# Performance work log

Measured on AMD Instinct MI355X. Metric: run time of the kernel, lower is better.

The kernel has to match this reference:

```python
import jax, jax.numpy as jnp
import numpy as np

# dims: L layers, D d_model, H heads, DH head_dim, DFF ffn, V vocab, BLK nf4 blocksize
L, D, H, DH, DFF, V, BLK = 2, 2048, 16, 128, 5504, 32000, 64
B, S, C, T = 4, 1000, 7, 45

# bitsandbytes NF4 codebook (fixed 16 quantiles of N(0,1), normalized to [-1,1])
NF4 = jnp.array([-1.0, -0.6961928009986877, -0.5250730514526367, -0.39491748809814453,
                 -0.28444138169288635, -0.18477343022823334, -0.09105003625154495, 0.0,
                 0.07958029955625534, 0.16093020141124725, 0.24611230194568634,
                 0.3379152417182922, 0.44070982933044434, 0.5626170039176941,
                 0.7229568362236023, 1.0], dtype=jnp.float32)


def _dequant(idx, scale):
    # idx: [out, in] int in [0,16); scale: [out, in//BLK] per-block absmax
    o, i = idx.shape
    return (NF4[idx].reshape(o, i // BLK, BLK) * scale[:, :, None]).reshape(o, i)


def _rmsnorm(h, w, eps=1e-5):
    return h * jax.lax.rsqrt(jnp.mean(h * h, axis=-1, keepdims=True) + eps) * w


def _rot_half(x):
    x1, x2 = jnp.split(x, 2, axis=-1)
    return jnp.concatenate([-x2, x1], axis=-1)


def _llama_fwd(token_ids, embed, wq_idx, wq_scale, wk_idx, wk_scale, wv_idx, wv_scale,
               wo_idx, wo_scale, wg_idx, wg_scale, wu_idx, wu_scale, wd_idx, wd_scale,
               ln1_w, ln2_w, lnf_w):
    Bt, St = token_ids.shape
    h = embed[token_ids]  # [B,S,D]
    # rotary embeddings
    inv = 1.0 / (10000.0 ** (jnp.arange(0, DH, 2, dtype=jnp.float32) / DH))
    ang = jnp.arange(St, dtype=jnp.float32)[:, None] * inv[None, :]  # [S, DH/2]
    emb_ang = jnp.concatenate([ang, ang], axis=-1)  # [S, DH]
    cos, sin = jnp.cos(emb_ang), jnp.sin(emb_ang)
    mask = jnp.where(jnp.tril(jnp.ones((St, St), dtype=bool)), 0.0, -1e9)  # causal
    for l in range(L):
        xn = _rmsnorm(h, ln1_w[l])
        q = (xn @ _dequant(wq_idx[l], wq_scale[l]).T).reshape(Bt, St, H, DH).transpose(0, 2, 1, 3)
        k = (xn @ _dequant(wk_idx[l], wk_scale[l]).T).reshape(Bt, St, H, DH).transpose(0, 2, 1, 3)
        v = (xn @ _dequant(wv_idx[l], wv_scale[l]).T).reshape(Bt, St, H, DH).transpose(0, 2, 1, 3)
        q = q * cos + _rot_half(q) * sin
        k = k * cos + _rot_half(k) * sin
        att = jax.nn.softmax(jnp.einsum('bhqd,bhkd->bhqk', q, k) / np.float32(np.sqrt(DH)) + mask, axis=-1)
        ctx = jnp.einsum('bhqk,bhkd->bhqd', att, v).transpose(0, 2, 1, 3).reshape(Bt, St, D)
        h = h + ctx @ _dequant(wo_idx[l], wo_scale[l]).T
        xn = _rmsnorm(h, ln2_w[l])
        g = xn @ _dequant(wg_idx[l], wg_scale[l]).T
        u = xn @ _dequant(wu_idx[l], wu_scale[l]).T
        h = h + (jax.nn.silu(g) * u) @ _dequant(wd_idx[l], wd_scale[l]).T
    # hidden_states[-1].mean(dim=1)
    return _rmsnorm(h, lnf_w).mean(axis=1)


def setup_inputs() -> dict:
    key = jax.random.key(0)
    ks = jax.random.split(key, 20)
    ridx = lambda k, shp: jax.random.randint(k, shp, 0, 16, dtype=jnp.int32)
    rsc = lambda k, shp: jax.random.uniform(k, shp, minval=0.01, maxval=0.03, dtype=jnp.float32)
    return {
        'x': jax.random.normal(ks[0], (B, C, T), dtype=jnp.float32),
        'token_ids': jax.random.randint(ks[1], (B, S), 0, V, dtype=jnp.int32),
        'embed': jax.random.normal(ks[2], (V, D), dtype=jnp.float32) * 0.02,
        'wq_idx': ridx(ks[3], (L, D, D)), 'wq_scale': rsc(ks[4], (L, D, D // BLK)),
        'wk_idx': ridx(ks[5], (L, D, D)), 'wk_scale': rsc(ks[6], (L, D, D // BLK)),
        'wv_idx': ridx(ks[7], (L, D, D)), 'wv_scale': rsc(ks[8], (L, D, D // BLK)),
        'wo_idx': ridx(ks[9], (L, D, D)), 'wo_scale': rsc(ks[10], (L, D, D // BLK)),
        'wg_idx': ridx(ks[11], (L, DFF, D)), 'wg_scale': rsc(ks[12], (L, DFF, D // BLK)),
        'wu_idx': ridx(ks[13], (L, DFF, D)), 'wu_scale': rsc(ks[14], (L, DFF, D // BLK)),
        'wd_idx': ridx(ks[15], (L, D, DFF)), 'wd_scale': rsc(ks[16], (L, D, DFF // BLK)),
        'ln1_w': jnp.ones((L, D), dtype=jnp.float32),
        'ln2_w': jnp.ones((L, D), dtype=jnp.float32),
        'lnf_w': jnp.ones((D,), dtype=jnp.float32),
        'proj_w': jax.random.normal(ks[17], (D, T), dtype=jnp.float32) * 0.05,
        'proj_b': jnp.zeros((D,), dtype=jnp.float32),
    }


def reference(x, token_ids, embed, wq_idx, wq_scale, wk_idx, wk_scale, wv_idx, wv_scale,
              wo_idx, wo_scale, wg_idx, wg_scale, wu_idx, wu_scale, wd_idx, wd_scale,
              ln1_w, ln2_w, lnf_w, proj_w, proj_b):
    # NF4-quantized Llama-style causal LM forward + mean pool over sequence
    e_text = _llama_fwd(token_ids, embed, wq_idx, wq_scale, wk_idx, wk_scale, wv_idx, wv_scale,
                        wo_idx, wo_scale, wg_idx, wg_scale, wu_idx, wu_scale, wd_idx, wd_scale,
                        ln1_w, ln2_w, lnf_w)  # [B, D]
    # series branch: channel-mean -> linear -> L2 normalize
    series_mean = x.mean(axis=1)  # [B, T]
    series_emb = series_mean @ proj_w.T + proj_b  # [B, D]
    series_emb = series_emb / jnp.maximum(jnp.linalg.norm(series_emb, axis=-1, keepdims=True), 1e-12)
    return e_text + series_emb
```

## Files before the change

kernel.cpp:

```cpp
#include <hip/hip_runtime.h>
#include <hip/hip_bf16.h>

#define L_N 2
#define D_ 2048
#define H_ 16
#define DH_ 128
#define DFF_ 5504
#define B_ 4
#define S_ 1000
#define C_ 7
#define T_ 45
#define M_ 4000

typedef short bf16x8 __attribute__((ext_vector_type(8)));
typedef float f32x4 __attribute__((ext_vector_type(4)));

__constant__ float NF4_TAB[16] = {
  -1.0f, -0.6961928009986877f, -0.5250730514526367f, -0.39491748809814453f,
  -0.28444138169288635f, -0.18477343022823334f, -0.09105003625154495f, 0.0f,
  0.07958029955625534f, 0.16093020141124725f, 0.24611230194568634f,
  0.3379152417182922f, 0.44070982933044434f, 0.5626170039176941f,
  0.7229568362236023f, 1.0f };

__device__ __forceinline__ unsigned short f2bf(float f) {
  unsigned int u = __float_as_uint(f);
  u += 0x7fffu + ((u >> 16) & 1u);
  return (unsigned short)(u >> 16);
}
__device__ __forceinline__ float bf2f(unsigned short u) {
  return __uint_as_float(((unsigned int)u) << 16);
}
__device__ __forceinline__ f32x4 zero4() { f32x4 z; z[0]=0.f; z[1]=0.f; z[2]=0.f; z[3]=0.f; return z; }
__device__ __forceinline__ f32x4 mfma16(bf16x8 a, bf16x8 b, f32x4 c) {
  return __builtin_amdgcn_mfma_f32_16x16x32_bf16(a, b, c, 0, 0, 0);
}

typedef __attribute__((address_space(3))) unsigned int lds_u32;
typedef const __attribute__((address_space(1))) unsigned int glb_u32;
__device__ __forceinline__ void gload16(const void* g, void* l) {
  __builtin_amdgcn_global_load_lds((glb_u32*)g, (lds_u32*)l, 16, 0, 0);
}

__global__ void rope_tables(float* __restrict__ cosT, float* __restrict__ sinT) {
  int s = blockIdx.x, d = threadIdx.x;
  int j = d & 63;
  float inv = expf(-(float)j * (9.210340371976184f / 64.f));
  float ang = (float)s * inv;
  cosT[s * DH_ + d] = cosf(ang);
  sinT[s * DH_ + d] = sinf(ang);
}

__global__ __launch_bounds__(256) void embed_gather(const int* __restrict__ tok,
    const float* __restrict__ emb, float* __restrict__ h) {
  int row = blockIdx.x;
  int tk = tok[row];
  const float4* src = reinterpret_cast<const float4*>(emb + (size_t)tk * D_);
  float4* dst = reinterpret_cast<float4*>(h + (size_t)row * D_);
  dst[threadIdx.x] = src[threadIdx.x];
  dst[threadIdx.x + 256] = src[threadIdx.x + 256];
}

__global__ __launch_bounds__(256) void rmsnorm_k(const float* __restrict__ h,
    const float* __restrict__ w, unsigned short* __restrict__ out) {
  const int row = blockIdx.x, t = threadIdx.x;
  const float* hp = h + (size_t)row * D_;
  float4 a = *reinterpret_cast<const float4*>(&hp[t * 8]);
  float4 b = *reinterpret_cast<const float4*>(&hp[t * 8 + 4]);
  float ss = a.x*a.x + a.y*a.y + a.z*a.z + a.w*a.w
           + b.x*b.x + b.y*b.y + b.z*b.z + b.w*b.w;
#pragma unroll
  for (int m = 1; m < 64; m <<= 1) ss += __shfl_xor(ss, m);
  __shared__ float red[4];
  if ((t & 63) == 0) red[t >> 6] = ss;
  __syncthreads();
  float tot = red[0] + red[1] + red[2] + red[3];
  float rs = rsqrtf(tot * (1.0f / D_) + 1e-5f);
  float4 wa = *reinterpret_cast<const float4*>(&w[t * 8]);
  float4 wb = *reinterpret_cast<const float4*>(&w[t * 8 + 4]);
  unsigned r0 = (unsigned)f2bf(a.x*rs*wa.x) | ((unsigned)f2bf(a.y*rs*wa.y) << 16);
  unsigned r1 = (unsigned)f2bf(a.z*rs*wa.z) | ((unsigned)f2bf(a.w*rs*wa.w) << 16);
  unsigned r2 = (unsigned)f2bf(b.x*rs*wb.x) | ((unsigned)f2bf(b.y*rs*wb.y) << 16);
  unsigned r3 = (unsigned)f2bf(b.z*rs*wb.z) | ((unsigned)f2bf(b.w*rs*wb.w) << 16);
  int4 ov; ov.x = (int)r0; ov.y = (int)r1; ov.z = (int)r2; ov.w = (int)r3;
  *reinterpret_cast<int4*>(&out[(size_t)row * D_ + t * 8]) = ov;
}

__global__ __launch_bounds__(256) void dequant_k(const int* __restrict__ idx,
    const float* __restrict__ sc, unsigned short* __restrict__ out, int K) {
  __shared__ float nf4[16];
  const int t = threadIdx.x;
  if (t < 16) nf4[t] = NF4_TAB[t];
  __syncthreads();
  const int row = blockIdx.y;
  const int k0 = blockIdx.x * 2048 + t * 8;
  if (k0 >= K) return;
  const size_t base = (size_t)row * K + k0;
  int4 a = *reinterpret_cast<const int4*>(&idx[base]);
  int4 b = *reinterpret_cast<const int4*>(&idx[base + 4]);
  float s = sc[(size_t)row * (K >> 6) + (k0 >> 6)];
  unsigned r0 = (unsigned)f2bf(nf4[a.x & 15] * s) | ((unsigned)f2bf(nf4[a.y & 15] * s) << 16);
  unsigned r1 = (unsigned)f2bf(nf4[a.z & 15] * s) | ((unsigned)f2bf(nf4[a.w & 15] * s) << 16);
  unsigned r2 = (unsigned)f2bf(nf4[b.x & 15] * s) | ((unsigned)f2bf(nf4[b.y & 15] * s) << 16);
  unsigned r3 = (unsigned)f2bf(nf4[b.z & 15] * s) | ((unsigned)f2bf(nf4[b.w & 15] * s) << 16);
  int4 ov; ov.x = (int)r0; ov.y = (int)r1; ov.z = (int)r2; ov.w = (int)r3;
  *reinterpret_cast<int4*>(&out[base]) = ov;
}

template<int MODE>
__global__ __launch_bounds__(256) void gemm_bf16(
    const unsigned short* __restrict__ A,
    const unsigned short* __restrict__ Bw,
    int Mdim, int N, int K, int nx,
    void* outp, const unsigned short* gin) {
  __shared__ unsigned short A_lds[2][128 * 64];
  __shared__ unsigned short B_lds[2][128 * 64];
  const int t = threadIdx.x;
  const int lane = t & 63, wid = t >> 6;

  const int nwg = gridDim.x;
  const int bid = blockIdx.x;
  const int wg = (bid & 7) * (nwg >> 3) + (bid >> 3);
  const int n0 = (wg % nx) * 128;
  const int m0 = (wg / nx) * 128;

  const int wm = (wid >> 1) * 64, wn = (wid & 1) * 64;
  const int lr = lane & 15, lg = lane >> 4;
  const int lrow = lane >> 3;
  const int lslot = (((lane & 7) ^ lrow) << 4);
  const int rswz = (lr & 7) << 4;

  f32x4 acc[4][4];
#pragma unroll
  for (int i = 0; i < 4; ++i)
#pragma unroll
    for (int j = 0; j < 4; ++j) acc[i][j] = zero4();

  const int kT = K >> 6;
  const size_t rowb = (size_t)(K * 2);

  auto stage = [&](int kt, int b) {
#pragma unroll
    for (int c0 = 0; c0 < 4; ++c0) {
      const int c = wid + 4 * c0;
      int gr = m0 + c * 8 + lrow;
      gr = gr < Mdim ? gr : Mdim - 1;
      gload16((const char*)A + (size_t)gr * rowb + kt * 128 + lslot,
              (char*)&A_lds[b][0] + c * 1024);
      const int nr = n0 + c * 8 + lrow;
      gload16((const char*)Bw + (size_t)nr * rowb + kt * 128 + lslot,
              (char*)&B_lds[b][0] + c * 1024);
    }
  };

  stage(0, 0);
  __syncthreads();

  for (int kt = 0; kt < kT; ++kt) {
    const int cur = kt & 1;
    if (kt + 1 < kT) stage(kt + 1, cur ^ 1);
#pragma unroll
    for (int ks = 0; ks < 2; ++ks) {
      bf16x8 af[4], bfr[4];
      const int cb = (ks * 64 + lg * 16) ^ rswz;
#pragma unroll
      for (int i = 0; i < 4; ++i) {
        af[i]  = *reinterpret_cast<const bf16x8*>(
                   (const char*)&A_lds[cur][0] + (wm + i * 16 + lr) * 128 + cb);
        bfr[i] = *reinterpret_cast<const bf16x8*>(
                   (const char*)&B_lds[cur][0] + (wn + i * 16 + lr) * 128 + cb);
      }
      __builtin_amdgcn_s_setprio(1);
#pragma unroll
      for (int mi = 0; mi < 4; ++mi)
#pragma unroll
        for (int ni = 0; ni < 4; ++ni)
          acc[mi][ni] = mfma16(af[mi], bfr[ni], acc[mi][ni]);
      __builtin_amdgcn_s_setprio(0);
    }
    __syncthreads();
  }

#pragma unroll
  for (int mi = 0; mi < 4; ++mi) {
#pragma unroll
    for (int r = 0; r < 4; ++r) {
      int gm = m0 + wm + mi * 16 + lg * 4 + r;
      if (gm >= Mdim) continue;
#pragma unroll
      for (int ni = 0; ni < 4; ++ni) {
        int gn = n0 + wn + ni * 16 + lr;
        float v = acc[mi][ni][r];
        if (MODE == 0) {
          ((unsigned short*)outp)[(size_t)gm * N + gn] = f2bf(v);
        } else if (MODE == 1) {
          int b = gm / S_, s = gm - b * S_;
          int hh = gn >> 7, d = gn & 127;
          ((unsigned short*)outp)[(((size_t)(b * H_ + hh) * S_ + s) << 7) + d] = f2bf(v);
        } else if (MODE == 2) {
          float g = bf2f(gin[(size_t)gm * N + gn]);
          float sg = g / (1.f + __expf(-g));
          ((unsigned short*)outp)[(size_t)gm * N + gn] = f2bf(sg * v);
        } else {
          ((float*)outp)[(size_t)gm * N + gn] += v;
        }
      }
    }
  }
}

__global__ __launch_bounds__(256) void rope_apply(unsigned short* __restrict__ qb,
    unsigned short* __restrict__ kb, const float* __restrict__ cosT,
    const float* __restrict__ sinT) {
  size_t i = (size_t)blockIdx.x * 256 + threadIdx.x;
  int d = (int)(i & 63);
  size_t row = i >> 6;
  int s = (int)(row % S_);
  size_t base = row * DH_;
  float c = cosT[s * DH_ + d], sn = sinT[s * DH_ + d];
  float q0 = bf2f(qb[base + d]), q1 = bf2f(qb[base + d + 64]);
  qb[base + d]      = f2bf(q0 * c - q1 * sn);
  qb[base + d + 64] = f2bf(q1 * c + q0 * sn);
  float k0 = bf2f(kb[base + d]), k1 = bf2f(kb[base + d + 64]);
  kb[base + d]      = f2bf(k0 * c - k1 * sn);
  kb[base + d + 64] = f2bf(k1 * c + k0 * sn);
}

__global__ __launch_bounds__(256) void vtrans_k(const unsigned short* __restrict__ vb,
    unsigned short* __restrict__ vt) {
  __shared__ unsigned int tile[64][33];
  const int t = threadIdx.x;
  const int s0 = blockIdx.x * 64, d0 = blockIdx.y * 64, bh = blockIdx.z;
#pragma unroll
  for (int j = 0; j < 2; ++j) {
    int idx = t + 256 * j;
    int s_r = idx >> 3, c8 = (idx & 7) << 3;
    int srow = s0 + s_r; srow = srow < S_ ? srow : S_ - 1;
    int4 v = *reinterpret_cast<const int4*>(&vb[((size_t)bh * S_ + srow) * DH_ + d0 + c8]);
    tile[s_r][(c8 >> 1) + 0] = (unsigned)v.x;
    tile[s_r][(c8 >> 1) + 1] = (unsigned)v.y;
    tile[s_r][(c8 >> 1) + 2] = (unsigned)v.z;
    tile[s_r][(c8 >> 1) + 3] = (unsigned)v.w;
  }
  __syncthreads();
#pragma unroll
  for (int j = 0; j < 2; ++j) {
    int idx = t + 256 * j;
    int d_r = idx >> 3, s8 = (idx & 7) << 3;
    unsigned r[8];
#pragma unroll
    for (int e = 0; e < 8; ++e) {
      unsigned wv = tile[s8 + e][d_r >> 1];
      r[e] = (d_r & 1) ? (wv >> 16) : (wv & 0xffffu);
    }
    int4 ov;
    ov.x = (int)(r[0] | (r[1] << 16));
    ov.y = (int)(r[2] | (r[3] << 16));
    ov.z = (int)(r[4] | (r[5] << 16));
    ov.w = (int)(r[6] | (r[7] << 16));
    *reinterpret_cast<int4*>(&vt[((size_t)(bh * 128 + d0 + d_r)) * 1024 + s0 + s8]) = ov;
  }
}

__global__ __launch_bounds__(512, 4) void attn2_k(const unsigned short* __restrict__ qg,
    const unsigned short* __restrict__ kg, const unsigned short* __restrict__ vtg,
    unsigned short* __restrict__ ctx) {
  __shared__ unsigned short K_lds[64 * 128];
  __shared__ unsigned short VT_lds[128 * 64];
  const int t = threadIdx.x, lane = t & 63, w = t >> 6;
  const int lr = lane & 15, lg = lane >> 4;
  const int bh = blockIdx.x, qt = blockIdx.y;
  const int q0 = qt * 128;
  const int b = bh >> 4, hh = bh & 15;
  const size_t kbase2 = (size_t)bh * S_ * DH_ * 2;
  const int q_idx = q0 + w * 16 + lr;
  const int swz = (lr & 7) << 4;

  bf16x8 qf[4];
#pragma unroll
  for (int ks = 0; ks < 4; ++ks) {
    bf16x8 z;
#pragma unroll
    for (int e = 0; e < 8; ++e) z[e] = 0;
    if (q_idx < S_)
      z = *reinterpret_cast<const bf16x8*>(
            (const char*)qg + kbase2 + (size_t)q_idx * 256 + ks * 64 + lg * 16);
    qf[ks] = z;
  }
  float mst = -1e30f, lst = 0.f;
  f32x4 cacc[8];
#pragma unroll
  for (int f = 0; f < 8; ++f) cacc[f] = zero4();

  const int q_hi = (q0 + 127 < S_) ? q0 + 127 : S_ - 1;
  const int nt = q_hi / 64 + 1;
  const int wq_max = q0 + w * 16 + 15;

  for (int kt = 0; kt < nt; ++kt) {
    const int kv0 = kt * 64;
    __syncthreads();
#pragma unroll
    for (int j = 0; j < 2; ++j) {
      const int chunk = w + 8 * j;
      int krow = chunk * 4 + (lane >> 4);
      int kcolb = (lane & 15) << 4;
      int gr = kv0 + krow; gr = gr < S_ ? gr : S_ - 1;
      gload16((const char*)kg + kbase2 + (size_t)gr * 256 + (kcolb ^ ((krow & 7) << 4)),
              (char*)K_lds + chunk * 1024);
      int vrow = chunk * 8 + (lane >> 3);
      int vcolb = (lane & 7) << 4;
      gload16((const char*)vtg + ((size_t)(bh * 128 + vrow) * 1024 + kv0) * 2 + (vcolb ^ ((vrow & 7) << 4)),
              (char*)VT_lds + chunk * 1024);
    }
    __syncthreads();
    if (kv0 > wq_max) continue;

    f32x4 sacc[4];
#pragma unroll
    for (int c = 0; c < 4; ++c) sacc[c] = zero4();
#pragma unroll
    for (int ks = 0; ks < 4; ++ks) {
#pragma unroll
      for (int c = 0; c < 4; ++c) {
        bf16x8 kf = *reinterpret_cast<const bf16x8*>(
            &K_lds[(c * 16 + lr) * 128 + (((ks * 64 + lg * 16) ^ swz) >> 1)]);
        sacc[c] = mfma16(kf, qf[ks], sacc[c]);
      }
    }
    float p[4][4];
    float mx = -1e30f;
#pragma unroll
    for (int c = 0; c < 4; ++c)
#pragma unroll
      for (int r = 0; r < 4; ++r) {
        int kv = kv0 + c * 16 + lg * 4 + r;
        float v = sacc[c][r] * 0.08838834764831845f;
        if (kv > q_idx || kv >= S_) v = -1e30f;
        p[c][r] = v;
        mx = fmaxf(mx, v);
      }
    mx = fmaxf(mx, __shfl_xor(mx, 16));
    mx = fmaxf(mx, __shfl_xor(mx, 32));
    float mn = fmaxf(mst, mx);
    float corr = __expf(mst - mn);
    mst = mn;
    float rs = 0.f;
#pragma unroll
    for (int c = 0; c < 4; ++c)
#pragma unroll
      for (int r = 0; r < 4; ++r) {
        float e = __expf(p[c][r] - mn);
        p[c][r] = e;
        rs += e;
      }
    rs += __shfl_xor(rs, 16);
    rs += __shfl_xor(rs, 32);
    lst = lst * corr + rs;
#pragma unroll
    for (int f = 0; f < 8; ++f)
#pragma unroll
      for (int r = 0; r < 4; ++r) cacc[f][r] *= corr;

    unsigned pk01[4], pk23[4];
#pragma unroll
    for (int c = 0; c < 4; ++c) {
      pk01[c] = (unsigned)f2bf(p[c][0]) | ((unsigned)f2bf(p[c][1]) << 16);
      pk23[c] = (unsigned)f2bf(p[c][2]) | ((unsigned)f2bf(p[c][3]) << 16);
    }
#pragma unroll
    for (int ks = 0; ks < 2; ++ks) {
      unsigned bu[4];
#pragma unroll
      for (int jj = 0; jj < 4; ++jj) {
        const int srcl = ((lg & 1) * 2 + (jj >> 1)) * 16 + lr;
        unsigned lo = (unsigned)__shfl((int)((jj & 1) ? pk23[2 * ks]     : pk01[2 * ks]),     srcl);
        unsigned hi = (unsigned)__shfl((int)((jj & 1) ? pk23[2 * ks + 1] : pk01[2 * ks + 1]), srcl);
        bu[jj] = (lg >= 2) ? hi : lo;
      }
      union { unsigned u[4]; bf16x8 v; } pb;
      pb.u[0] = bu[0]; pb.u[1] = bu[1]; pb.u[2] = bu[2]; pb.u[3] = bu[3];
#pragma unroll
      for (int f = 0; f < 8; ++f) {
        bf16x8 vtf = *reinterpret_cast<const bf16x8*>(
            &VT_lds[(f * 16 + lr) * 64 + (((ks * 64 + lg * 16) ^ swz) >> 1)]);
        cacc[f] = mfma16(vtf, pb.v, cacc[f]);
      }
    }
  }

  if (q_idx < S_) {
    float inv = 1.f / lst;
    unsigned short* cp = ctx + ((size_t)(b * S_ + q_idx)) * D_ + hh * 128;
#pragma unroll
    for (int f = 0; f < 8; ++f) {
      unsigned lo = (unsigned)f2bf(cacc[f][0] * inv) | ((unsigned)f2bf(cacc[f][1] * inv) << 16);
      unsigned hi = (unsigned)f2bf(cacc[f][2] * inv) | ((unsigned)f2bf(cacc[f][3] * inv) << 16);
      uint2 ov; ov.x = lo; ov.y = hi;
      *reinterpret_cast<uint2*>(cp + f * 16 + lg * 4) = ov;
    }
  }
}

__global__ __launch_bounds__(256) void meanpool(const unsigned short* __restrict__ xn,
    float* __restrict__ out) {
  int d = blockIdx.x * 256 + threadIdx.x;
  int b = blockIdx.y;
  const unsigned short* p = xn + (size_t)b * S_ * D_ + d;
  float s = 0.f;
  for (int i = 0; i < S_; ++i) s += bf2f(p[(size_t)i * D_]);
  out[(size_t)b * D_ + d] = s * (1.f / S_);
}

__global__ __launch_bounds__(256) void series_k(const float* __restrict__ x,
    const float* __restrict__ pw, const float* __restrict__ pb, float* out) {
  __shared__ float sm[T_];
  __shared__ float emb[D_];
  __shared__ float red[4];
  int b = blockIdx.x, t = threadIdx.x;
  if (t < T_) {
    float s = 0.f;
    for (int c = 0; c < C_; ++c) s += x[((size_t)b * C_ + c) * T_ + t];
    sm[t] = s * (1.f / C_);
  }
  __syncthreads();
  float ssq = 0.f;
#pragma unroll
  for (int j = 0; j < D_ / 256; ++j) {
    int d = j * 256 + t;
    float e = pb[d];
    for (int tt = 0; tt < T_; ++tt) e += sm[tt] * pw[(size_t)d * T_ + tt];
    emb[d] = e;
    ssq += e * e;
  }
#pragma unroll
  for (int m = 1; m < 64; m <<= 1) ssq += __shfl_xor(ssq, m);
  if ((t & 63) == 0) red[t >> 6] = ssq;
  __syncthreads();
  float tot = red[0] + red[1] + red[2] + red[3];
  float inv = 1.f / fmaxf(sqrtf(tot), 1e-12f);
#pragma unroll
  for (int j = 0; j < D_ / 256; ++j) {
    int d = j * 256 + t;
    out[(size_t)b * D_ + d] += emb[d] * inv;
  }
}

extern "C" void kernel_launch(void* const* d_in, const int* in_sizes, int n_in,
                              void* d_out, int out_size, void* d_ws, size_t ws_size,
                              hipStream_t stream) {
  const float* x      = (const float*)d_in[0];
  const int*   tok    = (const int*)d_in[1];
  const float* embedw = (const float*)d_in[2];
  const int*   wq_idx = (const int*)d_in[3];
  const float* wq_sc  = (const float*)d_in[4];
  const int*   wk_idx = (const int*)d_in[5];
  const float* wk_sc  = (const float*)d_in[6];
  const int*   wv_idx = (const int*)d_in[7];
  const float* wv_sc  = (const float*)d_in[8];
  const int*   wo_idx = (const int*)d_in[9];
  const float* wo_sc  = (const float*)d_in[10];
  const int*   wg_idx = (const int*)d_in[11];
  const float* wg_sc  = (const float*)d_in[12];
  const int*   wu_idx = (const int*)d_in[13];
  const float* wu_sc  = (const float*)d_in[14];
  const int*   wd_idx = (const int*)d_in[15];
  const float* wd_sc  = (const float*)d_in[16];
  const float* ln1    = (const float*)d_in[17];
  const float* ln2    = (const float*)d_in[18];
  const float* lnf    = (const float*)d_in[19];
  const float* projw  = (const float*)d_in[20];
  const float* projb  = (const float*)d_in[21];
  float* out = (float*)d_out;
  (void)in_sizes; (void)n_in; (void)out_size; (void)ws_size;

  char* wsp = (char*)d_ws;
  size_t off = 0;
  auto alloc = [&](size_t bytes) -> void* {
    void* p = wsp + off; off += (bytes + 255) & ~(size_t)255; return p; };
  float* cosT = (float*)alloc((size_t)S_ * DH_ * 4);
  float* sinT = (float*)alloc((size_t)S_ * DH_ * 4);
  float* hbuf = (float*)alloc((size_t)M_ * D_ * 4);
  unsigned short* xn  = (unsigned short*)alloc((size_t)M_ * D_ * 2);
  unsigned short* qb  = (unsigned short*)alloc((size_t)B_ * H_ * S_ * DH_ * 2);
  unsigned short* kb  = (unsigned short*)alloc((size_t)B_ * H_ * S_ * DH_ * 2);
  unsigned short* vb  = (unsigned short*)alloc((size_t)B_ * H_ * S_ * DH_ * 2);
  unsigned short* wdeq = (unsigned short*)alloc((size_t)DFF_ * D_ * 2);
  unsigned short* ctx = xn;
  unsigned short* gbuf = qb;
  unsigned short* vt  = wdeq;

  rope_tables<<<S_, DH_, 0, stream>>>(cosT, sinT);
  embed_gather<<<M_, 256, 0, stream>>>(tok, embedw, hbuf);

  const int nxAtt = D_ / 128;
  const int nxMlp = DFF_ / 128;
  const int my = (M_ + 127) / 128;
  const dim3 gAtt(nxAtt * my);
  const dim3 gMlp(nxMlp * my);
  const dim3 dqD(1, D_), dqF(1, DFF_), dqK(3, D_);

  for (int l = 0; l < L_N; ++l) {
    const int*   wqi = wq_idx + (size_t)l * D_ * D_;
    const float* wqs = wq_sc + (size_t)l * D_ * (D_ / 64);
    const int*   wki = wk_idx + (size_t)l * D_ * D_;
    const float* wks = wk_sc + (size_t)l * D_ * (D_ / 64);
    const int*   wvi = wv_idx + (size_t)l * D_ * D_;
    const float* wvs = wv_sc + (size_t)l * D_ * (D_ / 64);
    const int*   woi = wo_idx + (size_t)l * D_ * D_;
    const float* wos = wo_sc + (size_t)l * D_ * (D_ / 64);
    const int*   wgi = wg_idx + (size_t)l * DFF_ * D_;
    const float* wgs = wg_sc + (size_t)l * DFF_ * (D_ / 64);
    const int*   wui = wu_idx + (size_t)l * DFF_ * D_;
    const float* wus = wu_sc + (size_t)l * DFF_ * (D_ / 64);
    const int*   wdi = wd_idx + (size_t)l * D_ * DFF_;
    const float* wds = wd_sc + (size_t)l * D_ * (DFF_ / 64);

    rmsnorm_k<<<M_, 256, 0, stream>>>(hbuf, ln1 + l * D_, xn);
    dequant_k<<<dqD, 256, 0, stream>>>(wqi, wqs, wdeq, D_);
    gemm_bf16<1><<<gAtt, 256, 0, stream>>>(xn, wdeq, M_, D_, D_, nxAtt, qb, nullptr);
    dequant_k<<<dqD, 256, 0, stream>>>(wki, wks, wdeq, D_);
    gemm_bf16<1><<<gAtt, 256, 0, stream>>>(xn, wdeq, M_, D_, D_, nxAtt, kb, nullptr);
    dequant_k<<<dqD, 256, 0, stream>>>(wvi, wvs, wdeq, D_);
    gemm_bf16<1><<<gAtt, 256, 0, stream>>>(xn, wdeq, M_, D_, D_, nxAtt, vb, nullptr);
    rope_apply<<<(B_ * H_ * S_ * 64) / 256, 256, 0, stream>>>(qb, kb, cosT, sinT);
    vtrans_k<<<dim3(16, 2, B_ * H_), 256, 0, stream>>>(vb, vt);
    attn2_k<<<dim3(B_ * H_, 8), 512, 0, stream>>>(qb, kb, vt, ctx);
    dequant_k<<<dqD, 256, 0, stream>>>(woi, wos, wdeq, D_);
    gemm_bf16<3><<<gAtt, 256, 0, stream>>>(ctx, wdeq, M_, D_, D_, nxAtt, hbuf, nullptr);
    rmsnorm_k<<<M_, 256, 0, stream>>>(hbuf, ln2 + l * D_, xn);
    dequant_k<<<dqF, 256, 0, stream>>>(wgi, wgs, wdeq, D_);
    gemm_bf16<0><<<gMlp, 256, 0, stream>>>(xn, wdeq, M_, DFF_, D_, nxMlp, gbuf, nullptr);
    dequant_k<<<dqF, 256, 0, stream>>>(wui, wus, wdeq, D_);
    gemm_bf16<2><<<gMlp, 256, 0, stream>>>(xn, wdeq, M_, DFF_, D_, nxMlp, gbuf, gbuf);
    dequant_k<<<dqK, 256, 0, stream>>>(wdi, wds, wdeq, DFF_);
    gemm_bf16<3><<<gAtt, 256, 0, stream>>>(gbuf, wdeq, M_, D_, DFF_, nxAtt, hbuf, nullptr);
  }

  rmsnorm_k<<<M_, 256, 0, stream>>>(hbuf, lnf, xn);
  meanpool<<<dim3(D_ / 256, B_), 256, 0, stream>>>(xn, out);
  series_k<<<B_, 256, 0, stream>>>(x, projw, projb, out);
}
```

Before: 1.457 ms.

## Fuse QKV projections into one GEMM and batch NF4 dequant launches

The Wq, Wk and Wv dequantized weights are stacked into one buffer and projected with a single GEMM of width 3*D. Its epilogue scatters each column group into separate q, k and v head-major regions. Dequantization of several weight matrices now happens in one batched launch (QKV+O, gate+up), which needs a larger dequant workspace and a separate V-transpose buffer. The GEMM template also gains a single-buffered LDS variant, used for the gate projection, that trades prefetch overlap for less shared memory.

```diff
diff --git a/kernel.cpp b/kernel.cpp
--- a/kernel.cpp
+++ b/kernel.cpp
@@ -85,35 +85,38 @@
   *reinterpret_cast<int4*>(&out[(size_t)row * D_ + t * 8]) = ov;
 }
 
-__global__ __launch_bounds__(256) void dequant_k(const int* __restrict__ idx,
-    const float* __restrict__ sc, unsigned short* __restrict__ out, int K) {
+struct DqJob { const int* idx; const float* sc; unsigned short* out; };
+struct DqBatch { DqJob j[4]; };
+
+__global__ __launch_bounds__(256) void dequant_batch(DqBatch bt, int K) {
   __shared__ float nf4[16];
   const int t = threadIdx.x;
   if (t < 16) nf4[t] = NF4_TAB[t];
   __syncthreads();
+  const DqJob jb = bt.j[blockIdx.z];
   const int row = blockIdx.y;
   const int k0 = blockIdx.x * 2048 + t * 8;
   if (k0 >= K) return;
   const size_t base = (size_t)row * K + k0;
-  int4 a = *reinterpret_cast<const int4*>(&idx[base]);
-  int4 b = *reinterpret_cast<const int4*>(&idx[base + 4]);
-  float s = sc[(size_t)row * (K >> 6) + (k0 >> 6)];
+  int4 a = *reinterpret_cast<const int4*>(&jb.idx[base]);
+  int4 b = *reinterpret_cast<const int4*>(&jb.idx[base + 4]);
+  float s = jb.sc[(size_t)row * (K >> 6) + (k0 >> 6)];
   unsigned r0 = (unsigned)f2bf(nf4[a.x & 15] * s) | ((unsigned)f2bf(nf4[a.y & 15] * s) << 16);
   unsigned r1 = (unsigned)f2bf(nf4[a.z & 15] * s) | ((unsigned)f2bf(nf4[a.w & 15] * s) << 16);
   unsigned r2 = (unsigned)f2bf(nf4[b.x & 15] * s) | ((unsigned)f2bf(nf4[b.y & 15] * s) << 16);
   unsigned r3 = (unsigned)f2bf(nf4[b.z & 15] * s) | ((unsigned)f2bf(nf4[b.w & 15] * s) << 16);
   int4 ov; ov.x = (int)r0; ov.y = (int)r1; ov.z = (int)r2; ov.w = (int)r3;
-  *reinterpret_cast<int4*>(&out[base]) = ov;
-}
-
-template<int MODE>
+  *reinterpret_cast<int4*>(&jb.out[base]) = ov;
+}
+
+template<int MODE, int DBUF>
 __global__ __launch_bounds__(256) void gemm_bf16(
     const unsigned short* __restrict__ A,
     const unsigned short* __restrict__ Bw,
     int Mdim, int N, int K, int nx,
     void* outp, const unsigned short* gin) {
-  __shared__ unsigned short A_lds[2][128 * 64];
-  __shared__ unsigned short B_lds[2][128 * 64];
+  __shared__ unsigned short A_lds[(DBUF + 1) * 128 * 64];
+  __shared__ unsigned short B_lds[(DBUF + 1) * 128 * 64];
   const int t = threadIdx.x;
   const int lane = t & 63, wid = t >> 6;
 
@@ -145,19 +148,13 @@
       int gr = m0 + c * 8 + lrow;
       gr = gr < Mdim ? gr : Mdim - 1;
       gload16((const char*)A + (size_t)gr * rowb + kt * 128 + lslot,
-              (char*)&A_lds[b][0] + c * 1024);
+              (char*)&A_lds[0] + b * 16384 + c * 1024);
       const int nr = n0 + c * 8 + lrow;
       gload16((const char*)Bw + (size_t)nr * rowb + kt * 128 + lslot,
-              (char*)&B_lds[b][0] + c * 1024);
+              (char*)&B_lds[0] + b * 16384 + c * 1024);
     }
   };
-
-  stage(0, 0);
-  __syncthreads();
-
-  for (int kt = 0; kt < kT; ++kt) {
-    const int cur = kt & 1;
-    if (kt + 1 < kT) stage(kt + 1, cur ^ 1);
+  auto compute = [&](int cur) {
 #pragma unroll
     for (int ks = 0; ks < 2; ++ks) {
       bf16x8 af[4], bfr[4];
@@ -165,9 +162,9 @@
 #pragma unroll
       for (int i = 0; i < 4; ++i) {
         af[i]  = *reinterpret_cast<const bf16x8*>(
-                   (const char*)&A_lds[cur][0] + (wm + i * 16 + lr) * 128 + cb);
+                   (const char*)&A_lds[0] + cur * 16384 + (wm + i * 16 + lr) * 128 + cb);
         bfr[i] = *reinterpret_cast<const bf16x8*>(
-                   (const char*)&B_lds[cur][0] + (wn + i * 16 + lr) * 128 + cb);
+                   (const char*)&B_lds[0] + cur * 16384 + (wn + i * 16 + lr) * 128 + cb);
       }
       __builtin_amdgcn_s_setprio(1);
 #pragma unroll
@@ -177,7 +174,24 @@
           acc[mi][ni] = mfma16(af[mi], bfr[ni], acc[mi][ni]);
       __builtin_amdgcn_s_setprio(0);
     }
+  };
+
+  if (DBUF) {
+    stage(0, 0);
     __syncthreads();
+    for (int kt = 0; kt < kT; ++kt) {
+      const int cur = kt & 1;
+      if (kt + 1 < kT) stage(kt + 1, cur ^ 1);
+      compute(cur);
+      __syncthreads();
+    }
+  } else {
+    for (int kt = 0; kt < kT; ++kt) {
+      stage(kt, 0);
+      __syncthreads();
+      compute(0);
+      __syncthreads();
+    }
   }
 
 #pragma unroll
@@ -193,9 +207,11 @@
         if (MODE == 0) {
           ((unsigned short*)outp)[(size_t)gm * N + gn] = f2bf(v);
         } else if (MODE == 1) {
-          int b = gm / S_, s = gm - b * S_;
-          int hh = gn >> 7, d = gn & 127;
-          ((unsigned short*)outp)[(((size_t)(b * H_ + hh) * S_ + s) << 7) + d] = f2bf(v);
+          const int which = gn >> 11;
+          const int hh = (gn >> 7) & 15, dd = gn & 127;
+          const int b = gm / S_, s = gm - b * S_;
+          ((unsigned short*)outp)[
+            (((size_t)which * (B_ * H_) + b * H_ + hh) * S_ + s) * DH_ + dd] = f2bf(v);
         } else if (MODE == 2) {
           float g = bf2f(gin[(size_t)gm * N + gn]);
           float sg = g / (1.f + __expf(-g));
@@ -479,60 +495,80 @@
   float* cosT = (float*)alloc((size_t)S_ * DH_ * 4);
   float* sinT = (float*)alloc((size_t)S_ * DH_ * 4);
   float* hbuf = (float*)alloc((size_t)M_ * D_ * 4);
-  unsigned short* xn  = (unsigned short*)alloc((size_t)M_ * D_ * 2);
-  unsigned short* qb  = (unsigned short*)alloc((size_t)B_ * H_ * S_ * DH_ * 2);
-  unsigned short* kb  = (unsigned short*)alloc((size_t)B_ * H_ * S_ * DH_ * 2);
-  unsigned short* vb  = (unsigned short*)alloc((size_t)B_ * H_ * S_ * DH_ * 2);
-  unsigned short* wdeq = (unsigned short*)alloc((size_t)DFF_ * D_ * 2);
-  unsigned short* ctx = xn;
-  unsigned short* gbuf = qb;
-  unsigned short* vt  = wdeq;
+  unsigned short* xn   = (unsigned short*)alloc((size_t)M_ * D_ * 2);
+  unsigned short* qkv  = (unsigned short*)alloc((size_t)3 * B_ * H_ * S_ * DH_ * 2);
+  unsigned short* wdeq = (unsigned short*)alloc((size_t)2 * DFF_ * D_ * 2);
+  unsigned short* vt   = (unsigned short*)alloc((size_t)B_ * H_ * DH_ * 1024 * 2);
+  const size_t NH = (size_t)B_ * H_ * S_ * DH_;
+  unsigned short* qb = qkv, *kb = qkv + NH, *vb = qkv + 2 * NH;
+  unsigned short* ctx  = xn;
+  unsigned short* gbuf = qkv;
 
   rope_tables<<<S_, DH_, 0, stream>>>(cosT, sinT);
   embed_gather<<<M_, 256, 0, stream>>>(tok, embedw, hbuf);
 
-  const int nxAtt = D_ / 128;
-  const int nxMlp = DFF_ / 128;
   const int my = (M_ + 127) / 128;
-  const dim3 gAtt(nxAtt * my);
-  const dim3 gMlp(nxMlp * my);
-  const dim3 dqD(1, D_), dqF(1, DFF_), dqK(3, D_);
+  const dim3 gQKV((3 * D_ / 128) * my);
+  const dim3 gAtt((D_ / 128) * my);
+  const dim3 gMlp((DFF_ / 128) * my);
+  const size_t DD = (size_t)D_ * D_;
+  const size_t FD = (size_t)DFF_ * D_;
 
   for (int l = 0; l < L_N; ++l) {
-    const int*   wqi = wq_idx + (size_t)l * D_ * D_;
+    const int*   wqi = wq_idx + (size_t)l * DD;
     const float* wqs = wq_sc + (size_t)l * D_ * (D_ / 64);
-    const int*   wki = wk_idx + (size_t)l * D_ * D_;
+    const int*   wki = wk_idx + (size_t)l * DD;
     const float* wks = wk_sc + (size_t)l * D_ * (D_ / 64);
-    const int*   wvi = wv_idx + (size_t)l * D_ * D_;
+    const int*   wvi = wv_idx + (size_t)l * DD;
     const float* wvs = wv_sc + (size_t)l * D_ * (D_ / 64);
-    const int*   woi = wo_idx + (size_t)l * D_ * D_;
+    const int*   woi = wo_idx + (size_t)l * DD;
     const float* wos = wo_sc + (size_t)l * D_ * (D_ / 64);
-    const int*   wgi = wg_idx + (size_t)l * DFF_ * D_;
+    const int*   wgi = wg_idx + (size_t)l * FD;
     const float* wgs = wg_sc + (size_t)l * DFF_ * (D_ / 64);
-    const int*   wui = wu_idx + (size_t)l * DFF_ * D_;
+    const int*   wui = wu_idx + (size_t)l * FD;
     const float* wus = wu_sc + (size_t)l * DFF_ * (D_ / 64);
-    const int*   wdi = wd_idx + (size_t)l * D_ * DFF_;
+    const int*   wdi = wd_idx + (size_t)l * FD;
     const float* wds = wd_sc + (size_t)l * D_ * (DFF_ / 64);
 
     rmsnorm_k<<<M_, 256, 0, stream>>>(hbuf, ln1 + l * D_, xn);
-    dequant_k<<<dqD, 256, 0, stream>>>(wqi, wqs, wdeq, D_);
-    gemm_bf16<1><<<gAtt, 256, 0, stream>>>(xn, wdeq, M_, D_, D_, nxAtt, qb, nullptr);
-    dequant_k<<<dqD, 256, 0, stream>>>(wki, wks, wdeq, D_);
-    gemm_bf16<1><<<gAtt, 256, 0, stream>>>(xn, wdeq, M_, D_, D_, nxAtt, kb, nullptr);
-    dequant_k<<<dqD, 256, 0, stream>>>(wvi, wvs, wdeq, D_);
-    gemm_bf16<1><<<gAtt, 256, 0, stream>>>(xn, wdeq, M_, D_, D_, nxAtt, vb, nullptr);
+
+    {
+      DqBatch bt;
+      bt.j[0] = { wqi, wqs, wdeq };
+      bt.j[1] = { wki, wks, wdeq + DD };
+      bt.j[2] = { wvi, wvs, wdeq + 2 * DD };
+      bt.j[3] = { woi, wos, wdeq + 3 * DD };
+      dequant_batch<<<dim3(1, D_, 4), 256, 0, stream>>>(bt, D_);
+    }
+    gemm_bf16<1, 1><<<gQKV, 256, 0, stream>>>(xn, wdeq, M_, 3 * D_, D_, 3 * D_ / 128,
+                                              qkv, nullptr);
     rope_apply<<<(B_ * H_ * S_ * 64) / 256, 256, 0, stream>>>(qb, kb, cosT, sinT);
     vtrans_k<<<dim3(16, 2, B_ * H_), 256, 0, stream>>>(vb, vt);
     attn2_k<<<dim3(B_ * H_, 8), 512, 0, stream>>>(qb, kb, vt, ctx);
-    dequant_k<<<dqD, 256, 0, stream>>>(woi, wos, wdeq, D_);
-    gemm_bf16<3><<<gAtt, 256, 0, stream>>>(ctx, wdeq, M_, D_, D_, nxAtt, hbuf, nullptr);
+    gemm_bf16<3, 1><<<gAtt, 256, 0, stream>>>(ctx, wdeq + 3 * DD, M_, D_, D_, D_ / 128,
+                                              hbuf, nullptr);
     rmsnorm_k<<<M_, 256, 0, stream>>>(hbuf, ln2 + l * D_, xn);
-    dequant_k<<<dqF, 256, 0, stream>>>(wgi, wgs, wdeq, D_);
-    gemm_bf16<0><<<gMlp, 256, 0, stream>>>(xn, wdeq, M_, DFF_, D_, nxMlp, gbuf, nullptr);
-    dequant_k<<<dqF, 256, 0, stream>>>(wui, wus, wdeq, D_);
-    gemm_bf16<2><<<gMlp, 256, 0, stream>>>(xn, wdeq, M_, DFF_, D_, nxMlp, gbuf, gbuf);
-    dequant_k<<<dqK, 256, 0, stream>>>(wdi, wds, wdeq, DFF_);
-    gemm_bf16<3><<<gAtt, 256, 0, stream>>>(gbuf, wdeq, M_, D_, DFF_, nxAtt, hbuf, nullptr);
+
+    {
+      DqBatch bt;
+      bt.j[0] = { wgi, wgs, wdeq };
+      bt.j[1] = { wui, wus, wdeq + FD };
+      bt.j[2] = bt.j[0]; bt.j[3] = bt.j[0];
+      dequant_batch<<<dim3(1, DFF_, 2), 256, 0, stream>>>(bt, D_);
+    }
+    gemm_bf16<0, 0><<<gMlp, 256, 0, stream>>>(xn, wdeq, M_, DFF_, D_, DFF_ / 128,
+                                              gbuf, nullptr);
+    gemm_bf16<2, 1><<<gMlp, 256, 0, stream>>>(xn, wdeq + FD, M_, DFF_, D_, DFF_ / 128,
+                                              gbuf, gbuf);
+
+    {
+      DqBatch bt;
+      bt.j[0] = { wdi, wds, wdeq };
+      bt.j[1] = bt.j[0]; bt.j[2] = bt.j[0]; bt.j[3] = bt.j[0];
+      dequant_batch<<<dim3(3, D_, 1), 256, 0, stream>>>(bt, DFF_);
+    }
+    gemm_bf16<3, 1><<<gAtt, 256, 0, stream>>>(gbuf, wdeq, M_, D_, DFF_, D_ / 128,
+                                              hbuf, nullptr);
   }
 
   rmsnorm_k<<<M_, 256, 0, stream>>>(hbuf, lnf, xn);
```

Result: no change. 1.462 ms (+0.3%).
